# Performance work log

Measured on AMD Instinct MI355X. Metric: run time of the kernel, lower is better.

Reference implementation:

```python
import jax, jax.numpy as jnp
import numpy as np

H = 1024      # hidden_dim
NH = 16       # num_heads
HD = H // NH  # head_dim
FFN = 4096
EPS = 1e-5


def setup_inputs() -> dict:
    key = jax.random.key(0)
    ks = jax.random.split(key, 12)
    s = 0.02
    return {
        "x": jax.random.normal(ks[0], (2, 2048, H), dtype=jnp.float32),
        "w_qkv": jax.random.normal(ks[1], (H, 3 * H), dtype=jnp.float32) * s,
        "b_qkv": jnp.zeros((3 * H,), dtype=jnp.float32),
        "w_out": jax.random.normal(ks[2], (H, H), dtype=jnp.float32) * s,
        "b_out": jnp.zeros((H,), dtype=jnp.float32),
        "ln1_g": jnp.ones((H,), dtype=jnp.float32),
        "ln1_b": jnp.zeros((H,), dtype=jnp.float32),
        "ln2_g": jnp.ones((H,), dtype=jnp.float32),
        "ln2_b": jnp.zeros((H,), dtype=jnp.float32),
        "w1": jax.random.normal(ks[3], (H, FFN), dtype=jnp.float32) * s,
        "b1": jnp.zeros((FFN,), dtype=jnp.float32),
        "w2": jax.random.normal(ks[4], (FFN, H), dtype=jnp.float32) * s,
        "b2": jnp.zeros((H,), dtype=jnp.float32),
    }


def _layernorm(x, g, b):
    mu = jnp.mean(x, axis=-1, keepdims=True)
    var = jnp.mean(jnp.square(x - mu), axis=-1, keepdims=True)
    return (x - mu) * jax.lax.rsqrt(var + EPS) * g + b


def reference(x, w_qkv, b_qkv, w_out, b_out, ln1_g, ln1_b, ln2_g, ln2_b, w1, b1, w2, b2):
    B, S, _ = x.shape
    # pre-LN attention branch
    h = _layernorm(x, ln1_g, ln1_b)
    qkv = h @ w_qkv + b_qkv                       # (B,S,3H)
    qkv = qkv.reshape(B, S, 3, NH, HD).transpose(2, 0, 3, 1, 4)
    q, k, v = qkv[0], qkv[1], qkv[2]              # (B,NH,S,HD)
    scores = jnp.einsum("bhqd,bhkd->bhqk", q, k) / jnp.sqrt(jnp.float32(HD))
    causal = jnp.triu(jnp.ones((S, S), dtype=bool), k=1)
    scores = jnp.where(causal, -jnp.inf, scores)
    attn = jax.nn.softmax(scores, axis=-1)
    out = jnp.einsum("bhqk,bhkd->bhqd", attn, v)  # (B,NH,S,HD)
    out = out.transpose(0, 2, 1, 3).reshape(B, S, H)
    attn_out = out @ w_out + b_out
    x = x + attn_out
    # FFN branch
    h2 = _layernorm(x, ln2_g, ln2_b)
    ffn = jax.nn.gelu(h2 @ w1 + b1, approximate=False) @ w2 + b2
    return x + ffn
```

## Files before the change

kernel.cpp:

```cpp
#include <hip/hip_runtime.h>
#include <hip/hip_bf16.h>

typedef __bf16 bf16_t;
typedef __bf16 bf16x8 __attribute__((ext_vector_type(8)));
typedef __bf16 bf16x4 __attribute__((ext_vector_type(4)));
typedef __bf16 bf16x2 __attribute__((ext_vector_type(2)));
typedef float  f32x4  __attribute__((ext_vector_type(4)));

#define HDIM 1024
#define SEQ  2048
#define NHEAD 16
#define HEADD 64

__device__ __forceinline__ void gld_lds16(const void* g, void* l) {
  __builtin_amdgcn_global_load_lds(
      (const __attribute__((address_space(1))) unsigned int*)g,
      (__attribute__((address_space(3))) unsigned int*)l, 16, 0, 0);
}

__device__ __forceinline__ float fexp2(float x) {
#if __has_builtin(__builtin_amdgcn_exp2f)
  return __builtin_amdgcn_exp2f(x);
#else
  return exp2f(x);
#endif
}

__global__ __launch_bounds__(256) void ln_kernel(const float* __restrict__ x,
                                                 const float* __restrict__ gam,
                                                 const float* __restrict__ bet,
                                                 bf16_t* __restrict__ out) {
  int row = blockIdx.x;
  int t = threadIdx.x;
  const float4* xr = (const float4*)(x + (size_t)row * HDIM);
  float4 v = xr[t];
  float s = v.x + v.y + v.z + v.w;
  float ss = v.x*v.x + v.y*v.y + v.z*v.z + v.w*v.w;
  #pragma unroll
  for (int o = 32; o > 0; o >>= 1) {
    s  += __shfl_xor(s, o);
    ss += __shfl_xor(ss, o);
  }
  __shared__ float red[8];
  int w = t >> 6;
  if ((t & 63) == 0) { red[w*2] = s; red[w*2+1] = ss; }
  __syncthreads();
  s  = red[0] + red[2] + red[4] + red[6];
  ss = red[1] + red[3] + red[5] + red[7];
  float mu  = s * (1.0f / HDIM);
  float var = ss * (1.0f / HDIM) - mu * mu;
  float rstd = rsqrtf(var + 1e-5f);
  float4 g4 = ((const float4*)gam)[t];
  float4 b4 = ((const float4*)bet)[t];
  bf16x4 o4;
  o4[0] = (bf16_t)((v.x - mu) * rstd * g4.x + b4.x);
  o4[1] = (bf16_t)((v.y - mu) * rstd * g4.y + b4.y);
  o4[2] = (bf16_t)((v.z - mu) * rstd * g4.z + b4.z);
  o4[3] = (bf16_t)((v.w - mu) * rstd * g4.w + b4.w);
  *(bf16x4*)(out + (size_t)row * HDIM + t * 4) = o4;
}

__global__ __launch_bounds__(256)
void transpose_all(const float* __restrict__ w_qkv, bf16_t* __restrict__ wqkvT,
                   const float* __restrict__ w_out, bf16_t* __restrict__ woutT,
                   const float* __restrict__ w1,    bf16_t* __restrict__ w1T,
                   const float* __restrict__ w2,    bf16_t* __restrict__ w2T) {
  int bid = blockIdx.x;
  const float* W; bf16_t* Wt; int Kd, Nd, nbx;
  if (bid < 768)        { W = w_qkv; Wt = wqkvT; Kd = 1024; Nd = 3072; nbx = 48; }
  else if (bid < 1024)  { bid -= 768;  W = w_out; Wt = woutT; Kd = 1024; Nd = 1024; nbx = 16; }
  else if (bid < 2048)  { bid -= 1024; W = w1;    Wt = w1T;   Kd = 1024; Nd = 4096; nbx = 64; }
  else                  { bid -= 2048; W = w2;    Wt = w2T;   Kd = 4096; Nd = 1024; nbx = 16; }
  int n0 = (bid % nbx) * 64, k0 = (bid / nbx) * 64;

  __shared__ float tile[64][65];
  int t = threadIdx.x;
  int tx = t & 15, ty = t >> 4;
  #pragma unroll
  for (int i = 0; i < 4; i++) {
    float4 v = *(const float4*)(W + (size_t)(k0 + ty + i*16) * Nd + n0 + tx*4);
    tile[ty + i*16][tx*4 + 0] = v.x;
    tile[ty + i*16][tx*4 + 1] = v.y;
    tile[ty + i*16][tx*4 + 2] = v.z;
    tile[ty + i*16][tx*4 + 3] = v.w;
  }
  __syncthreads();
  #pragma unroll
  for (int i = 0; i < 4; i++) {
    int r = ty + i*16;
    bf16x4 o4;
    o4[0] = (bf16_t)tile[tx*4 + 0][r];
    o4[1] = (bf16_t)tile[tx*4 + 1][r];
    o4[2] = (bf16_t)tile[tx*4 + 2][r];
    o4[3] = (bf16_t)tile[tx*4 + 3][r];
    *(bf16x4*)(Wt + (size_t)(n0 + r) * Kd + k0 + tx*4) = o4;
  }
}

__device__ __forceinline__ float gelu_fast(float x) {
  float y = 0.7978845608f * (x + 0.044715f * x * x * x);
  float u = fexp2(y * 2.885390082f);
  float th = 1.0f - 2.0f * __builtin_amdgcn_rcpf(u + 1.0f);
  return 0.5f * x * (1.0f + th);
}

__global__ __launch_bounds__(256)
void reduce2_kernel(const bf16_t* __restrict__ p0, const bf16_t* __restrict__ p1,
                    const float* __restrict__ bias, const float* __restrict__ resid,
                    float* __restrict__ out) {
  size_t base = ((size_t)blockIdx.x * 256 + threadIdx.x) * 8;
  bf16x8 a = *(const bf16x8*)(p0 + base);
  bf16x8 b = *(const bf16x8*)(p1 + base);
  int col = (int)(base & (HDIM - 1));
  float4 bi0 = *(const float4*)(bias + col);
  float4 bi1 = *(const float4*)(bias + col + 4);
  float4 r0 = *(const float4*)(resid + base);
  float4 r1 = *(const float4*)(resid + base + 4);
  float4 o0, o1;
  o0.x = (float)a[0] + (float)b[0] + bi0.x + r0.x;
  o0.y = (float)a[1] + (float)b[1] + bi0.y + r0.y;
  o0.z = (float)a[2] + (float)b[2] + bi0.z + r0.z;
  o0.w = (float)a[3] + (float)b[3] + bi0.w + r0.w;
  o1.x = (float)a[4] + (float)b[4] + bi1.x + r1.x;
  o1.y = (float)a[5] + (float)b[5] + bi1.y + r1.y;
  o1.z = (float)a[6] + (float)b[6] + bi1.z + r1.z;
  o1.w = (float)a[7] + (float)b[7] + bi1.w + r1.w;
  *(float4*)(out + base)     = o0;
  *(float4*)(out + base + 4) = o1;
}

template<int EPI, int BN, int BK, int WPEU, int SPLITK>
__global__ __launch_bounds__(256, WPEU)
void gemm_bt(const bf16_t* __restrict__ A, const bf16_t* __restrict__ Bt,
             const float* __restrict__ bias, const float* __restrict__ resid,
             void* __restrict__ outp, int M, int N, int K) {
  constexpr int NFRAG = BN / 32;
  constexpr int CH  = BK / 8;
  constexpr int SWZ = CH - 1;
  constexpr int RSH = (BK == 32) ? 1 : 0;
  constexpr int RPP = 256 / CH;
  __shared__ bf16_t As[2][128*BK];
  __shared__ bf16_t Bs[2][BN*BK];
  int t = threadIdx.x;
  int w = t >> 6, l = t & 63;
  int wr = w >> 1, wc = w & 1;

  int nbx = gridDim.x;
  int bid = blockIdx.y * nbx + blockIdx.x;
  int chunkx = (nbx * gridDim.y) >> 3;
  int nb = (bid & 7) * chunkx + (bid >> 3);
  int bm = nb / nbx, bn = nb % nbx;
  size_t m0 = (size_t)bm * 128, n0 = (size_t)bn * BN;

  const int KK = (SPLITK > 1) ? K / SPLITK : K;
  const size_t koff = (SPLITK > 1) ? (size_t)blockIdx.z * KK : 0;

  f32x4 acc[4][NFRAG];
  #pragma unroll
  for (int m = 0; m < 4; m++)
    #pragma unroll
    for (int n = 0; n < NFRAG; n++) acc[m][n] = (f32x4)(0.0f);

  int srow = t / CH;
  int scol = ((t & SWZ) ^ ((srow >> RSH) & SWZ)) * 8;
  int dsto = t * 8;
  const bf16_t* ag = A  + (m0 + srow) * K + koff + scol;
  const bf16_t* bg = Bt + (n0 + srow) * K + koff + scol;

  int lr = l & 15, lg = l >> 4;

  auto stage = [&](int buf, int k0) {
    #pragma unroll
    for (int p = 0; p < 128/RPP; p++)
      gld_lds16(ag + k0 + (size_t)(p*RPP)*K, &As[buf][dsto + p*RPP*BK]);
    #pragma unroll
    for (int p = 0; p < BN/RPP; p++)
      gld_lds16(bg + k0 + (size_t)(p*RPP)*K, &Bs[buf][dsto + p*RPP*BK]);
  };

  stage(0, 0);
  __syncthreads();
  int cur = 0;
  const int NK = KK / BK;
  for (int k = 0; k < NK; k++) {
    if (k + 1 < NK) stage(cur ^ 1, (k + 1) * BK);
    #pragma unroll
    for (int kk = 0; kk < BK/32; kk++) {
      bf16x8 af[4], bfr[NFRAG];
      #pragma unroll
      for (int m = 0; m < 4; m++) {
        int row = wr*64 + m*16 + lr;
        int off = row*BK*2 + (((kk*4 + lg) ^ ((row >> RSH) & SWZ)) << 4);
        af[m] = *(const bf16x8*)((const char*)&As[cur][0] + off);
      }
      #pragma unroll
      for (int n = 0; n < NFRAG; n++) {
        int row = wc*(BN/2) + n*16 + lr;
        int off = row*BK*2 + (((kk*4 + lg) ^ ((row >> RSH) & SWZ)) << 4);
        bfr[n] = *(const bf16x8*)((const char*)&Bs[cur][0] + off);
      }
      #pragma unroll
      for (int m = 0; m < 4; m++)
        #pragma unroll
        for (int n = 0; n < NFRAG; n++)
          acc[m][n] = __builtin_amdgcn_mfma_f32_16x16x32_bf16(af[m], bfr[n], acc[m][n], 0, 0, 0);
    }
    __syncthreads();
    cur ^= 1;
  }

  int r0 = (l >> 4) * 4, c0 = l & 15;
  bf16_t* pd = nullptr;
  if (EPI == 3)
    pd = (bf16_t*)(blockIdx.z == 0 ? outp : (void*)resid);
  #pragma unroll
  for (int m = 0; m < 4; m++) {
    #pragma unroll
    for (int n = 0; n < NFRAG; n++) {
      size_t row = m0 + wr*64 + m*16 + r0;
      size_t col = n0 + wc*(BN/2) + n*16 + c0;
      float bv = (EPI == 3) ? 0.0f : bias[col];
      #pragma unroll
      for (int r = 0; r < 4; r++) {
        float vv = acc[m][n][r] + bv;
        size_t idx = (row + r) * (size_t)N + col;
        if (EPI == 0) {
          ((bf16_t*)outp)[idx] = (bf16_t)vv;
        } else if (EPI == 1) {
          ((float*)outp)[idx] = vv + resid[idx];
        } else if (EPI == 2) {
          ((bf16_t*)outp)[idx] = (bf16_t)gelu_fast(vv);
        } else {
          pd[idx] = (bf16_t)vv;
        }
      }
    }
  }
}

__global__ __launch_bounds__(512, 4)
void attn_kernel(const bf16_t* __restrict__ qkv, bf16_t* __restrict__ out) {
  int idx = blockIdx.x;
  int half = idx >> 8;
  int sub = idx & 255;
  int qth = sub >> 5;
  int qt = half ? qth : (15 - qth);
  int bh = sub & 31;
  int b = bh >> 4, h = bh & 15;
  int t = threadIdx.x, w = t >> 6, l = t & 63;

  __shared__ bf16_t Ks[2][64*64];
  __shared__ bf16_t Vt[2][64*72];
  __shared__ bf16_t Ps[8][16*64];

  const size_t RS = 3 * HDIM;
  const bf16_t* qb = qkv + (size_t)b * SEQ * RS + h * HEADD;
  const bf16_t* kb = qb + HDIM;
  const bf16_t* vb = qb + 2 * HDIM;

  int lr = l & 15, lg = l >> 4;
  const float SCALE = 0.125f * 1.44269504f;

  bf16x8 qf[2];
  {
    size_t qrow = (size_t)qt * 128 + w * 16 + lr;
    qf[0] = *(const bf16x8*)(qb + qrow * RS + lg * 8);
    qf[1] = *(const bf16x8*)(qb + qrow * RS + 32 + lg * 8);
    #pragma unroll
    for (int i = 0; i < 8; i++) {
      qf[0][i] = (bf16_t)((float)qf[0][i] * SCALE);
      qf[1][i] = (bf16_t)((float)qf[1][i] * SCALE);
    }
  }

  f32x4 o[4];
  #pragma unroll
  for (int d = 0; d < 4; d++) o[d] = (f32x4)(0.0f);
  float m = -1e30f, lsum = 0.0f;

  int srow = t >> 3, scol = (t & 7) * 8;
  int Fv = ((scol >> 3) & 7) << 3;
  int nkt = 2 * qt + 2;

  const bf16_t* kg0 = kb + (size_t)srow * RS + scol;
  const bf16_t* vg0 = vb + (size_t)srow * RS + scol;

  bf16x8 kr = *(const bf16x8*)kg0;
  bf16x8 vr = *(const bf16x8*)vg0;

  int wrow0 = qt * 128 + w * 16;
  int qg = wrow0 + lr;
  bf16_t* pw = Ps[w];
  int psw = (lr & 7) << 4;
  int cur = 0;

  for (int kt = 0; kt < nkt; kt++) {
    {
      int ba = srow * 128 + scol * 2;
      int sw = (srow & 7) << 4;
      *(bf16x8*)((char*)Ks[cur] + (ba ^ sw)) = kr;
      int ksw = srow ^ Fv;
      bf16_t* vt = Vt[cur];
      #pragma unroll
      for (int i = 0; i < 8; i++)
        vt[(scol + i) * 72 + ksw] = vr[i];
    }
    if (kt + 1 < nkt) {
      kr = *(const bf16x8*)(kg0 + (size_t)(kt + 1) * 64 * RS);
      vr = *(const bf16x8*)(vg0 + (size_t)(kt + 1) * 64 * RS);
    }
    asm volatile("s_waitcnt lgkmcnt(0)" ::: "memory");
    __builtin_amdgcn_s_barrier();
    __builtin_amdgcn_sched_barrier(0);

    bool skipw = (kt * 64) > (wrow0 + 15);
    if (!skipw) {
      f32x4 sc[4];
      __builtin_amdgcn_s_setprio(1);
      #pragma unroll
      for (int kt2 = 0; kt2 < 4; kt2++) {
        sc[kt2] = (f32x4)(0.0f);
        #pragma unroll
        for (int kk = 0; kk < 2; kk++) {
          int row = kt2 * 16 + lr;
          int off = (row * 128 + kk * 64 + lg * 16) ^ ((row & 7) << 4);
          bf16x8 kf = *(const bf16x8*)((char*)Ks[cur] + off);
          sc[kt2] = __builtin_amdgcn_mfma_f32_16x16x32_bf16(kf, qf[kk], sc[kt2], 0, 0, 0);
        }
      }
      __builtin_amdgcn_s_setprio(0);
      if (kt * 64 + 63 > wrow0) {
        #pragma unroll
        for (int kt2 = 0; kt2 < 4; kt2++) {
          #pragma unroll
          for (int r = 0; r < 4; r++) {
            int kcol = kt*64 + kt2*16 + lg*4 + r;
            if (kcol > qg) sc[kt2][r] = -1e30f;
          }
        }
      }
      float tm0 = fmaxf(fmaxf(sc[0][0], sc[0][1]), fmaxf(sc[0][2], sc[0][3]));
      float tm1 = fmaxf(fmaxf(sc[1][0], sc[1][1]), fmaxf(sc[1][2], sc[1][3]));
      float tm2 = fmaxf(fmaxf(sc[2][0], sc[2][1]), fmaxf(sc[2][2], sc[2][3]));
      float tm3 = fmaxf(fmaxf(sc[3][0], sc[3][1]), fmaxf(sc[3][2], sc[3][3]));
      float tm = fmaxf(fmaxf(tm0, tm1), fmaxf(tm2, tm3));
      tm = fmaxf(tm, __shfl_xor(tm, 16));
      tm = fmaxf(tm, __shfl_xor(tm, 32));
      if (!__all(tm <= m + 8.0f)) {
        float nm = fmaxf(m, tm);
        float alpha = fexp2(m - nm);
        m = nm;
        lsum *= alpha;
        #pragma unroll
        for (int d = 0; d < 4; d++)
          #pragma unroll
          for (int r = 0; r < 4; r++) o[d][r] *= alpha;
      }
      #pragma unroll
      for (int kt2 = 0; kt2 < 4; kt2++) {
        float p0 = fexp2(sc[kt2][0] - m);
        float p1 = fexp2(sc[kt2][1] - m);
        float p2 = fexp2(sc[kt2][2] - m);
        float p3 = fexp2(sc[kt2][3] - m);
        lsum += (p0 + p1) + (p2 + p3);
        bf16x2 pa; pa[0] = (bf16_t)p0; pa[1] = (bf16_t)p1;
        bf16x2 pb; pb[0] = (bf16_t)p2; pb[1] = (bf16_t)p3;
        int base = lr * 128 + kt2 * 32 + lg * 8;
        *(bf16x2*)((char*)pw + ((base)     ^ psw)) = pa;
        *(bf16x2*)((char*)pw + ((base + 4) ^ psw)) = pb;
      }
      asm volatile("s_waitcnt lgkmcnt(0)" ::: "memory");
      __builtin_amdgcn_s_setprio(1);
      #pragma unroll
      for (int kk = 0; kk < 2; kk++) {
        int poff = (lr * 128 + kk * 64 + lg * 16) ^ psw;
        bf16x8 pf = *(const bf16x8*)((char*)pw + poff);
        #pragma unroll
        for (int dblk = 0; dblk < 4; dblk++) {
          int vrow = dblk * 16 + lr;
          int Fd = ((vrow >> 3) & 7) << 3;
          bf16x8 vf = *(const bf16x8*)(Vt[cur] + vrow * 72 + ((kk * 32 + lg * 8) ^ Fd));
          o[dblk] = __builtin_amdgcn_mfma_f32_16x16x32_bf16(vf, pf, o[dblk], 0, 0, 0);
        }
      }
      __builtin_amdgcn_s_setprio(0);
    }
    cur ^= 1;
  }

  lsum += __shfl_xor(lsum, 16);
  lsum += __shfl_xor(lsum, 32);
  float inv = 1.0f / lsum;

  bf16_t* ob = out + ((size_t)b * SEQ + qg) * HDIM + h * HEADD;
  #pragma unroll
  for (int dblk = 0; dblk < 4; dblk++) {
    bf16x4 q4;
    #pragma unroll
    for (int r = 0; r < 4; r++) q4[r] = (bf16_t)(o[dblk][r] * inv);
    *(bf16x4*)(ob + dblk * 16 + lg * 4) = q4;
  }
}

extern "C" void kernel_launch(void* const* d_in, const int* in_sizes, int n_in,
                              void* d_out, int out_size, void* d_ws, size_t ws_size,
                              hipStream_t stream) {
  (void)in_sizes; (void)n_in; (void)out_size; (void)ws_size;
  const float* x     = (const float*)d_in[0];
  const float* w_qkv = (const float*)d_in[1];
  const float* b_qkv = (const float*)d_in[2];
  const float* w_out = (const float*)d_in[3];
  const float* b_out = (const float*)d_in[4];
  const float* ln1_g = (const float*)d_in[5];
  const float* ln1_b = (const float*)d_in[6];
  const float* ln2_g = (const float*)d_in[7];
  const float* ln2_b = (const float*)d_in[8];
  const float* w1    = (const float*)d_in[9];
  const float* b1    = (const float*)d_in[10];
  const float* w2    = (const float*)d_in[11];
  const float* b2    = (const float*)d_in[12];
  float* out = (float*)d_out;

  char* ws = (char*)d_ws;
  size_t off = 0;
  auto alloc = [&](size_t bytes) -> void* {
    void* p = ws + off;
    off += (bytes + 255) & ~(size_t)255;
    return p;
  };
  bf16_t* wqkvT = (bf16_t*)alloc((size_t)3072*1024*2);
  bf16_t* woutT = (bf16_t*)alloc((size_t)1024*1024*2);
  bf16_t* w1T   = (bf16_t*)alloc((size_t)4096*1024*2);
  bf16_t* w2T   = (bf16_t*)alloc((size_t)1024*4096*2);
  bf16_t* ln1o  = (bf16_t*)alloc((size_t)4096*1024*2);
  bf16_t* qkvb  = (bf16_t*)alloc((size_t)4096*4096*2);
  bf16_t* attno = (bf16_t*)alloc((size_t)4096*1024*2);
  float*  x2    = (float*) alloc((size_t)4096*1024*4);
  bf16_t* h2 = ln1o;
  bf16_t* g  = qkvb;
  bf16_t* part0 = ln1o;
  bf16_t* part1 = attno;

  dim3 blk(256);
  transpose_all<<<3072, blk, 0, stream>>>(w_qkv, wqkvT, w_out, woutT, w1, w1T, w2, w2T);

  ln_kernel<<<4096, blk, 0, stream>>>(x, ln1_g, ln1_b, ln1o);
  gemm_bt<0,128,32,4,1><<<dim3(24, 32), blk, 0, stream>>>(ln1o, wqkvT, b_qkv, nullptr, qkvb, 4096, 3072, 1024);
  attn_kernel<<<512, dim3(512), 0, stream>>>(qkvb, attno);
  gemm_bt<1,64,64,2,1><<<dim3(16, 32), blk, 0, stream>>>(attno, woutT, b_out, x, x2, 4096, 1024, 1024);
  ln_kernel<<<4096, blk, 0, stream>>>(x2, ln2_g, ln2_b, h2);
  gemm_bt<2,128,32,4,1><<<dim3(32, 32), blk, 0, stream>>>(h2, w1T, b1, nullptr, g, 4096, 4096, 1024);
  gemm_bt<3,64,32,4,2><<<dim3(16, 32, 2), blk, 0, stream>>>(g, w2T, b2, (const float*)part1, part0, 4096, 1024, 4096);
  reduce2_kernel<<<2048, blk, 0, stream>>>(part0, part1, b2, x2, out);
}
```

Measured before the change: 226.7 us.

## Use 4-way split-K with 128-wide tiles for FFN down-projection

The final FFN down GEMM goes from 2-way split-K with 64-wide N tiles to 4-way split-K with 128-wide N tiles, keeping the grid at 1024 blocks. Each block now does a larger output tile over a shorter K range, which is meant to improve operand reuse. Two extra bf16 partial buffers reuse workspace regions whose data is no longer needed, and the reduce kernel now sums four partials. The trade-off is more partial-sum traffic and extra bf16 rounding from more partials.

Measured after the change: 219.1 us. -3.3%, faster.

```diff
diff --git a/kernel.cpp b/kernel.cpp
--- a/kernel.cpp
+++ b/kernel.cpp
@@ -105,26 +105,29 @@
 }
 
 __global__ __launch_bounds__(256)
-void reduce2_kernel(const bf16_t* __restrict__ p0, const bf16_t* __restrict__ p1,
+void reduce4_kernel(const bf16_t* __restrict__ p0, const bf16_t* __restrict__ p1,
+                    const bf16_t* __restrict__ p2, const bf16_t* __restrict__ p3,
                     const float* __restrict__ bias, const float* __restrict__ resid,
                     float* __restrict__ out) {
   size_t base = ((size_t)blockIdx.x * 256 + threadIdx.x) * 8;
   bf16x8 a = *(const bf16x8*)(p0 + base);
   bf16x8 b = *(const bf16x8*)(p1 + base);
+  bf16x8 c = *(const bf16x8*)(p2 + base);
+  bf16x8 d = *(const bf16x8*)(p3 + base);
   int col = (int)(base & (HDIM - 1));
   float4 bi0 = *(const float4*)(bias + col);
   float4 bi1 = *(const float4*)(bias + col + 4);
   float4 r0 = *(const float4*)(resid + base);
   float4 r1 = *(const float4*)(resid + base + 4);
   float4 o0, o1;
-  o0.x = (float)a[0] + (float)b[0] + bi0.x + r0.x;
-  o0.y = (float)a[1] + (float)b[1] + bi0.y + r0.y;
-  o0.z = (float)a[2] + (float)b[2] + bi0.z + r0.z;
-  o0.w = (float)a[3] + (float)b[3] + bi0.w + r0.w;
-  o1.x = (float)a[4] + (float)b[4] + bi1.x + r1.x;
-  o1.y = (float)a[5] + (float)b[5] + bi1.y + r1.y;
-  o1.z = (float)a[6] + (float)b[6] + bi1.z + r1.z;
-  o1.w = (float)a[7] + (float)b[7] + bi1.w + r1.w;
+  o0.x = ((float)a[0] + (float)b[0]) + ((float)c[0] + (float)d[0]) + bi0.x + r0.x;
+  o0.y = ((float)a[1] + (float)b[1]) + ((float)c[1] + (float)d[1]) + bi0.y + r0.y;
+  o0.z = ((float)a[2] + (float)b[2]) + ((float)c[2] + (float)d[2]) + bi0.z + r0.z;
+  o0.w = ((float)a[3] + (float)b[3]) + ((float)c[3] + (float)d[3]) + bi0.w + r0.w;
+  o1.x = ((float)a[4] + (float)b[4]) + ((float)c[4] + (float)d[4]) + bi1.x + r1.x;
+  o1.y = ((float)a[5] + (float)b[5]) + ((float)c[5] + (float)d[5]) + bi1.y + r1.y;
+  o1.z = ((float)a[6] + (float)b[6]) + ((float)c[6] + (float)d[6]) + bi1.z + r1.z;
+  o1.w = ((float)a[7] + (float)b[7]) + ((float)c[7] + (float)d[7]) + bi1.w + r1.w;
   *(float4*)(out + base)     = o0;
   *(float4*)(out + base + 4) = o1;
 }
@@ -133,7 +136,8 @@
 __global__ __launch_bounds__(256, WPEU)
 void gemm_bt(const bf16_t* __restrict__ A, const bf16_t* __restrict__ Bt,
              const float* __restrict__ bias, const float* __restrict__ resid,
-             void* __restrict__ outp, int M, int N, int K) {
+             void* __restrict__ outp, int M, int N, int K,
+             bf16_t* __restrict__ p2, bf16_t* __restrict__ p3) {
   constexpr int NFRAG = BN / 32;
   constexpr int CH  = BK / 8;
   constexpr int SWZ = CH - 1;
@@ -211,8 +215,12 @@
 
   int r0 = (l >> 4) * 4, c0 = l & 15;
   bf16_t* pd = nullptr;
-  if (EPI == 3)
-    pd = (bf16_t*)(blockIdx.z == 0 ? outp : (void*)resid);
+  if (EPI == 3) {
+    if (blockIdx.z == 0)      pd = (bf16_t*)outp;
+    else if (blockIdx.z == 1) pd = (bf16_t*)(void*)resid;
+    else if (blockIdx.z == 2) pd = p2;
+    else                      pd = p3;
+  }
   #pragma unroll
   for (int m = 0; m < 4; m++) {
     #pragma unroll
@@ -440,16 +448,18 @@
   bf16_t* g  = qkvb;
   bf16_t* part0 = ln1o;
   bf16_t* part1 = attno;
+  bf16_t* part2 = (bf16_t*)ws;
+  bf16_t* part3 = w1T;
 
   dim3 blk(256);
   transpose_all<<<3072, blk, 0, stream>>>(w_qkv, wqkvT, w_out, woutT, w1, w1T, w2, w2T);
 
   ln_kernel<<<4096, blk, 0, stream>>>(x, ln1_g, ln1_b, ln1o);
-  gemm_bt<0,128,32,4,1><<<dim3(24, 32), blk, 0, stream>>>(ln1o, wqkvT, b_qkv, nullptr, qkvb, 4096, 3072, 1024);
+  gemm_bt<0,128,32,4,1><<<dim3(24, 32), blk, 0, stream>>>(ln1o, wqkvT, b_qkv, nullptr, qkvb, 4096, 3072, 1024, nullptr, nullptr);
   attn_kernel<<<512, dim3(512), 0, stream>>>(qkvb, attno);
-  gemm_bt<1,64,64,2,1><<<dim3(16, 32), blk, 0, stream>>>(attno, woutT, b_out, x, x2, 4096, 1024, 1024);
+  gemm_bt<1,64,64,2,1><<<dim3(16, 32), blk, 0, stream>>>(attno, woutT, b_out, x, x2, 4096, 1024, 1024, nullptr, nullptr);
   ln_kernel<<<4096, blk, 0, stream>>>(x2, ln2_g, ln2_b, h2);
-  gemm_bt<2,128,32,4,1><<<dim3(32, 32), blk, 0, stream>>>(h2, w1T, b1, nullptr, g, 4096, 4096, 1024);
-  gemm_bt<3,64,32,4,2><<<dim3(16, 32, 2), blk, 0, stream>>>(g, w2T, b2, (const float*)part1, part0, 4096, 1024, 4096);
-  reduce2_kernel<<<2048, blk, 0, stream>>>(part0, part1, b2, x2, out);
-}
+  gemm_bt<2,128,32,4,1><<<dim3(32, 32), blk, 0, stream>>>(h2, w1T, b1, nullptr, g, 4096, 4096, 1024, nullptr, nullptr);
+  gemm_bt<3,128,32,4,4><<<dim3(8, 32, 4), blk, 0, stream>>>(g, w2T, b2, (const float*)part1, part0, 4096, 1024, 4096, part2, part3);
+  reduce4_kernel<<<2048, blk, 0, stream>>>(part0, part1, part2, part3, b2, x2, out);
+}
```
